# Performance work log

Measured on AMD Instinct MI355X. Metric: run time of the kernel, lower is better.

Reference implementation:

```python
import jax, jax.numpy as jnp
import numpy as np

B, N, C, NT = 32, 512, 32, 24   # batch, frames, channels-per-token, tokens
H, DH = 8, 48                   # heads, dim_head (DH % NT == 0 -> CS = 2)
E = H * DH                      # encode_dim = 384
IN = C * NT                     # in_dim = 768
OUT = 768                       # out_dim


def setup_inputs() -> dict:
    key = jax.random.key(0)
    ks = jax.random.split(key, 12)
    s = lambda fan_in: 1.0 / np.sqrt(fan_in)
    return {
        "x": jax.random.normal(ks[0], (B, N, C, NT), dtype=jnp.float32),
        "Wqkv_t": jax.random.uniform(ks[1], (IN, 3 * E), jnp.float32, -s(IN), s(IN)),
        "bqkv_t": jax.random.uniform(ks[2], (3 * E,), jnp.float32, -s(IN), s(IN)),
        "Wqkv_s": jax.random.uniform(ks[3], (IN, 3 * E), jnp.float32, -s(IN), s(IN)),
        "bqkv_s": jax.random.uniform(ks[4], (3 * E,), jnp.float32, -s(IN), s(IN)),
        "Wts": jax.random.uniform(ks[5], (2 * E, 2 * E), jnp.float32, -s(2 * E), s(2 * E)),
        "bts": jax.random.uniform(ks[6], (2 * E,), jnp.float32, -s(2 * E), s(2 * E)),
        "Wfc_t": jax.random.uniform(ks[7], (E, OUT), jnp.float32, -s(E), s(E)),
        "bfc_t": jax.random.uniform(ks[8], (OUT,), jnp.float32, -s(E), s(E)),
        "Wfc_s": jax.random.uniform(ks[9], (E, OUT), jnp.float32, -s(E), s(E)),
        "bfc_s": jax.random.uniform(ks[10], (OUT,), jnp.float32, -s(E), s(E)),
    }


def reference(x, Wqkv_t, bqkv_t, Wqkv_s, bqkv_s, Wts, bts, Wfc_t, bfc_t, Wfc_s, bfc_s):
    b, n, c, nt = x.shape
    cs = DH // nt  # channels per token inside a head (=2)
    xf = x.reshape(b, n, c * nt)                       # (b, n, in_dim)

    # --- temporal attention over the n (frame) axis ---
    qkv_t = (xf @ Wqkv_t + bqkv_t).reshape(b, n, 3, H, DH)
    qkv_t = jnp.transpose(qkv_t, (2, 0, 3, 1, 4))      # (3, b, H, n, DH)
    qt, kt, vt = qkv_t[0], qkv_t[1], qkv_t[2]
    attn_t = jax.nn.softmax(
        jnp.einsum('bhnd,bhmd->bhnm', qt, kt) / jnp.sqrt(jnp.float32(DH)), axis=-1)
    x_t = jnp.einsum('bhnm,bhmd->bnhd', attn_t, vt).reshape(b, n, E)

    # --- spatial attention over the nt (token) axis (note: unscaled, per source) ---
    qkv_s = (xf @ Wqkv_s + bqkv_s).reshape(b, n, 3, H, DH)
    qkv_s = jnp.transpose(qkv_s, (2, 0, 1, 3, 4)).reshape(3, b * n, H, cs, nt)
    qs, ks_, vs = qkv_s[0], qkv_s[1], qkv_s[2]         # (b*n, H, cs, nt)
    attn_s = jax.nn.softmax(jnp.einsum('ghct,ghcu->ghtu', qs, ks_), axis=-1)
    x_s = jnp.einsum('ghtu,ghcu->ghct', attn_s, vs)     # (b*n, H, cs, nt)
    x_s = x_s.reshape(b * n, H, cs * nt).reshape(b, n, E)

    # --- learned gating fusion ---
    alpha = jnp.concatenate([x_t, x_s], axis=-1).mean(axis=1, keepdims=True)  # (b,1,2E)
    alpha = (alpha @ Wts + bts).reshape(b, 1, E, 2)
    alpha = jax.nn.softmax(alpha, axis=-1)
    y = (x_t * alpha[:, :, :, 0]) @ Wfc_t + bfc_t + (x_s * alpha[:, :, :, 1]) @ Wfc_s + bfc_s
    return y  # dropout is identity in inference
```

## Files before the change

kernel.cpp:

```cpp
#include <hip/hip_runtime.h>
#include <hip/hip_bf16.h>


typedef __attribute__((ext_vector_type(8))) short s16x8;
typedef __attribute__((ext_vector_type(4))) float f32x4;

__device__ __forceinline__ float lo2f(uint u) { return __uint_as_float(u << 16); }
__device__ __forceinline__ float hi2f(uint u) { return __uint_as_float(u & 0xffff0000u); }
__device__ __forceinline__ ushort f2bu(float f) {
    union { __hip_bfloat16 h; ushort u; } c; c.h = __float2bfloat16(f); return c.u;
}
__device__ __forceinline__ uint pk2(float a, float b) {
    return (uint)f2bu(a) | ((uint)f2bu(b) << 16);
}
__device__ __forceinline__ void gload16(const void* g, void* l) {
    __builtin_amdgcn_global_load_lds((const __attribute__((address_space(1))) void*)g,
                                     (__attribute__((address_space(3))) void*)l, 16, 0, 0);
}

__global__ __launch_bounds__(256) void convert_bf16(
    const float* __restrict__ in, ushort* __restrict__ out)
{
    const int i = blockIdx.x * 256 + threadIdx.x;
    const float4* p = (const float4*)in + (size_t)i * 2;
    float4 a = p[0], b = p[1];
    uint4 o;
    o.x = pk2(a.x, a.y); o.y = pk2(a.z, a.w);
    o.z = pk2(b.x, b.y); o.w = pk2(b.z, b.w);
    ((uint4*)out)[i] = o;
}

__global__ __launch_bounds__(256) void concat_bias(
    const float* __restrict__ a, const float* __restrict__ b, float* __restrict__ o)
{
    const int i = blockIdx.x * 256 + threadIdx.x;
    o[i] = (i < 1152) ? a[i] : b[i - 1152];
}

__global__ __launch_bounds__(256) void transpose_w(
    const float* __restrict__ W, ushort* __restrict__ Bt,
    int K, int N, int Kt, int koff, int noff)
{
    __shared__ float t[32][33];
    const int k0 = blockIdx.x * 32, n0 = blockIdx.y * 32;
    const int r = threadIdx.x >> 3, cq = threadIdx.x & 7;
    float4 v = *(const float4*)(W + (size_t)(k0 + r) * N + n0 + cq * 4);
    t[r][cq * 4 + 0] = v.x; t[r][cq * 4 + 1] = v.y;
    t[r][cq * 4 + 2] = v.z; t[r][cq * 4 + 3] = v.w;
    __syncthreads();
    ushort4 o;
    o.x = f2bu(t[cq * 4 + 0][r]); o.y = f2bu(t[cq * 4 + 1][r]);
    o.z = f2bu(t[cq * 4 + 2][r]); o.w = f2bu(t[cq * 4 + 3][r]);
    *(ushort4*)(Bt + (size_t)(noff + n0 + r) * Kt + koff + k0 + cq * 4) = o;
}

template<int OUTBF16, int NBIAS>
__global__ __launch_bounds__(256, 2) void gemm128p(
    const ushort* __restrict__ A, const ushort* __restrict__ Bt,
    const float* __restrict__ bias0, const float* __restrict__ bias1,
    void* __restrict__ Cout, int M, int N, int K)
{
    __shared__ ushort smem[32768];
    const int tid = threadIdx.x;
    const int m0 = blockIdx.x * 128;
    const int n0 = blockIdx.y * 128;
    const int lane = tid & 63;
    const int wr = tid >> 7;
    const int wc = (tid >> 6) & 1;
    const int lr = lane & 15;
    const int g = lane >> 4;

    f32x4 acc[4][4];
#pragma unroll
    for (int i = 0; i < 4; ++i)
#pragma unroll
        for (int j = 0; j < 4; ++j) acc[i][j] = (f32x4){0.f, 0.f, 0.f, 0.f};

    int rowT[4], kqs[4];
#pragma unroll
    for (int i = 0; i < 4; ++i) {
        const int task = tid + 256 * i;
        rowT[i] = task >> 3;
        kqs[i] = (task & 7) ^ (rowT[i] & 7);
    }

    auto stage = [&](int buf, int k0) {
        ushort* dA = &smem[buf * 16384];
        ushort* dB = &smem[buf * 16384 + 8192];
#pragma unroll
        for (int i = 0; i < 4; ++i) {
            gload16(A + (size_t)(m0 + rowT[i]) * K + k0 + (kqs[i] << 3),
                    dA + (tid + 256 * i) * 8);
            gload16(Bt + (size_t)(n0 + rowT[i]) * K + k0 + (kqs[i] << 3),
                    dB + (tid + 256 * i) * 8);
        }
    };

    stage(0, 0);
    const int nt = K >> 6;
    for (int t = 0; t < nt; ++t) {
        const int cur = t & 1;
        if (t + 1 < nt) {
            stage(cur ^ 1, (t + 1) << 6);
            asm volatile("s_waitcnt vmcnt(8)" ::: "memory");
        } else {
            asm volatile("s_waitcnt vmcnt(0)" ::: "memory");
        }
        __builtin_amdgcn_sched_barrier(0);
        __builtin_amdgcn_s_barrier();
        __builtin_amdgcn_sched_barrier(0);

        const ushort* As = &smem[cur * 16384];
        const ushort* Bs = &smem[cur * 16384 + 8192];
#pragma unroll
        for (int half = 0; half < 2; ++half) {
            s16x8 af[4], bfv[4];
#pragma unroll
            for (int i = 0; i < 4; ++i) {
                const int row = wr * 64 + 16 * i + lr;
                af[i] = *(const s16x8*)&As[row * 64
                         + (((4 * half + g) ^ (row & 7)) << 3)];
            }
#pragma unroll
            for (int j = 0; j < 4; ++j) {
                const int row = wc * 64 + 16 * j + lr;
                bfv[j] = *(const s16x8*)&Bs[row * 64
                          + (((4 * half + g) ^ (row & 7)) << 3)];
            }
#pragma unroll
            for (int i = 0; i < 4; ++i)
#pragma unroll
                for (int j = 0; j < 4; ++j)
                    acc[i][j] = __builtin_amdgcn_mfma_f32_16x16x32_bf16(
                        af[i], bfv[j], acc[i][j], 0, 0, 0);
        }
        __builtin_amdgcn_sched_barrier(0);
        __builtin_amdgcn_s_barrier();
    }

    const int c0 = n0 + wc * 64 + lr;
    float bsum[4];
#pragma unroll
    for (int j = 0; j < 4; ++j) {
        bsum[j] = bias0[c0 + 16 * j];
        if (NBIAS == 2) bsum[j] += bias1[c0 + 16 * j];
    }
    const int r0 = m0 + wr * 64 + g * 4;
#pragma unroll
    for (int i = 0; i < 4; ++i) {
        const int row = r0 + 16 * i;
#pragma unroll
        for (int j = 0; j < 4; ++j) {
            const int col = c0 + 16 * j;
#pragma unroll
            for (int v = 0; v < 4; ++v) {
                const float val = acc[i][j][v] + bsum[j];
                if (OUTBF16)
                    ((ushort*)Cout)[(size_t)(row + v) * N + col] = f2bu(val);
                else
                    ((float*)Cout)[(size_t)(row + v) * N + col] = val;
            }
        }
    }
}

__global__ __launch_bounds__(256, 4) void attn_temporal(
    const ushort* __restrict__ qkv, ushort* __restrict__ xcat)
{
    const int wg = blockIdx.x;
    const int cx = wg & 7, rx = wg >> 3;
    const int id = ((rx >> 2) << 5) + 4 * cx + (rx & 3);
    const int qt = id & 3;
    const int h = (id >> 2) & 7;
    const int b = id >> 5;

    const int tid = threadIdx.x;
    const int w = tid >> 6;
    const int lane = tid & 63;
    const int lr = lane & 15;
    const int g = lane >> 4;

    __shared__ ushort Ks[64 * 64];
    __shared__ ushort Vt[48 * 64];
    __shared__ ushort Pl[4][32 * 72];
    uint* KsU = (uint*)Ks;
    uint* VtU = (uint*)Vt;

    ((uint4*)Ks)[tid] = make_uint4(0u, 0u, 0u, 0u);
    ((uint4*)Ks)[256 + tid] = make_uint4(0u, 0u, 0u, 0u);
    __syncthreads();

    const uint* qkvu = (const uint*)qkv;
    const int qrow0 = qt * 128 + w * 32;

    s16x8 qf[2][2];
#pragma unroll
    for (int n = 0; n < 2; ++n) {
        const size_t rb = (size_t)(b * 512 + qrow0 + 16 * n + lr) * 2304 + h * 48 + 8 * g;
        qf[n][0] = *(const s16x8*)(qkv + rb);
        qf[n][1] = (g < 2) ? *(const s16x8*)(qkv + rb + 32)
                           : (s16x8){0, 0, 0, 0, 0, 0, 0, 0};
    }

    int p_[3], du_[3];
#pragma unroll
    for (int i = 0; i < 3; ++i) {
        const int idx = tid + 256 * i;
        p_[i] = idx / 24;
        du_[i] = idx % 24;
    }
    uint rk[3][2], rv[3][2];

    auto stage_load = [&](int kv0) {
#pragma unroll
        for (int i = 0; i < 3; ++i) {
            const uint* s0 = qkvu + (size_t)(b * 512 + kv0 + 2 * p_[i]) * 1152
                                  + 192 + h * 24 + du_[i];
            rk[i][0] = s0[0];    rk[i][1] = s0[1152];
            rv[i][0] = s0[192];  rv[i][1] = s0[192 + 1152];
        }
    };
    auto stage_write = [&]() {
#pragma unroll
        for (int i = 0; i < 3; ++i) {
            const int p = p_[i], du = du_[i];
            KsU[(2 * p) * 32 + ((((du >> 2) ^ ((2 * p) & 7)) << 2) | (du & 3))] = rk[i][0];
            KsU[(2 * p + 1) * 32 + ((((du >> 2) ^ ((2 * p + 1) & 7)) << 2) | (du & 3))] = rk[i][1];
            const uint w0 = (rv[i][0] & 0xffffu) | (rv[i][1] << 16);
            const uint w1 = (rv[i][0] >> 16) | (rv[i][1] & 0xffff0000u);
            const int vb = (((p >> 2) ^ (du & 7)) << 2) | (p & 3);
            VtU[(2 * du) * 32 + vb] = w0;
            VtU[(2 * du + 1) * 32 + vb] = w1;
        }
    };

    f32x4 o[2][3];
#pragma unroll
    for (int mq = 0; mq < 2; ++mq)
#pragma unroll
        for (int nd = 0; nd < 3; ++nd) o[mq][nd] = (f32x4){0.f, 0.f, 0.f, 0.f};
    float mrun[2] = {-3.0e38f, -3.0e38f};
    float lsum[2] = {0.f, 0.f};
    float corrv[2];
    const float scale = 0.14433756729740643f;

    stage_load(0);
    stage_write();
    __syncthreads();

    for (int t = 0; t < 8; ++t) {
        if (t < 7) stage_load((t + 1) * 64);

        f32x4 sa[4][2];
#pragma unroll
        for (int m = 0; m < 4; ++m)
#pragma unroll
            for (int n = 0; n < 2; ++n) sa[m][n] = (f32x4){0.f, 0.f, 0.f, 0.f};
#pragma unroll
        for (int ks = 0; ks < 2; ++ks)
#pragma unroll
            for (int m = 0; m < 4; ++m) {
                s16x8 kf = *(const s16x8*)&Ks[(16 * m + lr) * 64
                                              + (((g + 4 * ks) ^ (lr & 7)) << 3)];
#pragma unroll
                for (int n = 0; n < 2; ++n)
                    sa[m][n] = __builtin_amdgcn_mfma_f32_16x16x32_bf16(
                        kf, qf[n][ks], sa[m][n], 0, 0, 0);
            }

#pragma unroll
        for (int n = 0; n < 2; ++n) {
            float tmax = -3.0e38f;
#pragma unroll
            for (int m = 0; m < 4; ++m)
#pragma unroll
                for (int v = 0; v < 4; ++v) tmax = fmaxf(tmax, sa[m][n][v]);
            tmax = fmaxf(tmax, __shfl_xor(tmax, 16));
            tmax = fmaxf(tmax, __shfl_xor(tmax, 32));
            float mnew = fmaxf(mrun[n], tmax * scale);
            float corr = __expf(mrun[n] - mnew);
            mrun[n] = mnew;
            float psum = 0.f;
#pragma unroll
            for (int m = 0; m < 4; ++m) {
                float p0 = __expf(fmaf(sa[m][n][0], scale, -mnew));
                float p1 = __expf(fmaf(sa[m][n][1], scale, -mnew));
                float p2 = __expf(fmaf(sa[m][n][2], scale, -mnew));
                float p3 = __expf(fmaf(sa[m][n][3], scale, -mnew));
                psum += (p0 + p1) + (p2 + p3);
                const int base = (16 * n + lr) * 72 + 16 * m + 4 * g;
                *(uint*)&Pl[w][base] = pk2(p0, p1);
                *(uint*)&Pl[w][base + 2] = pk2(p2, p3);
            }
            psum += __shfl_xor(psum, 16);
            psum += __shfl_xor(psum, 32);
            lsum[n] = lsum[n] * corr + psum;
            corrv[n] = corr;
        }

#pragma unroll
        for (int mq = 0; mq < 2; ++mq)
#pragma unroll
            for (int nd = 0; nd < 3; ++nd)
#pragma unroll
                for (int v = 0; v < 4; ++v) o[mq][nd][v] *= corrv[mq];

#pragma unroll
        for (int ks = 0; ks < 2; ++ks) {
            s16x8 vf[3];
#pragma unroll
            for (int nd = 0; nd < 3; ++nd)
                vf[nd] = *(const s16x8*)&Vt[(16 * nd + lr) * 64
                                            + (((g + 4 * ks) ^ (lr >> 1)) << 3)];
#pragma unroll
            for (int mq = 0; mq < 2; ++mq) {
                s16x8 pf = *(const s16x8*)&Pl[w][(16 * mq + lr) * 72 + 8 * g + 32 * ks];
#pragma unroll
                for (int nd = 0; nd < 3; ++nd)
                    o[mq][nd] = __builtin_amdgcn_mfma_f32_16x16x32_bf16(
                        vf[nd], pf, o[mq][nd], 0, 0, 0);
            }
        }
        __syncthreads();
        if (t < 7) stage_write();
        __syncthreads();
    }

#pragma unroll
    for (int mq = 0; mq < 2; ++mq) {
        const float li = 1.f / lsum[mq];
        const int qrow = qrow0 + 16 * mq + lr;
        ushort* dst = xcat + (size_t)(b * 512 + qrow) * 768 + h * 48;
#pragma unroll
        for (int nd = 0; nd < 3; ++nd) {
            uint2 o2;
            o2.x = pk2(o[mq][nd][0] * li, o[mq][nd][1] * li);
            o2.y = pk2(o[mq][nd][2] * li, o[mq][nd][3] * li);
            *(uint2*)(dst + 16 * nd + 4 * g) = o2;
        }
    }
}

__global__ __launch_bounds__(192) void attn_spatial(
    const ushort* __restrict__ qkv, ushort* __restrict__ xcat)
{
    const int g = blockIdx.x;
    __shared__ float row[1152];
    const uint* qkvu = (const uint*)qkv;
#pragma unroll
    for (int i = 0; i < 3; ++i) {
        int idx = threadIdx.x + 192 * i;
        uint u = qkvu[(size_t)g * 1152 + 576 + idx];
        row[2 * idx] = lo2f(u); row[2 * idx + 1] = hi2f(u);
    }
    __syncthreads();

    const int h = threadIdx.x / 24;
    const int t = threadIdx.x % 24;
    const float* q = &row[h * 48];
    const float* k = &row[384 + h * 48];
    const float* v = &row[768 + h * 48];
    const float q0 = q[t], q1 = q[24 + t];

    float s[24];
    float mx = -3.0e38f;
#pragma unroll
    for (int u = 0; u < 24; ++u) {
        s[u] = q0 * k[u] + q1 * k[24 + u];
        mx = fmaxf(mx, s[u]);
    }
    float l = 0.f;
#pragma unroll
    for (int u = 0; u < 24; ++u) { s[u] = __expf(s[u] - mx); l += s[u]; }
    const float inv = 1.f / l;
    float o0 = 0.f, o1 = 0.f;
#pragma unroll
    for (int u = 0; u < 24; ++u) {
        o0 = fmaf(s[u], v[u], o0);
        o1 = fmaf(s[u], v[24 + u], o1);
    }
    ushort* dst = xcat + (size_t)g * 768 + 384 + h * 48;
    dst[t] = f2bu(o0 * inv);
    dst[24 + t] = f2bu(o1 * inv);
}

__global__ __launch_bounds__(256) void colsum(
    const ushort* __restrict__ xcat, float* __restrict__ partial)
{
    const int b = blockIdx.x, ch = blockIdx.y, part = blockIdx.z;
    const int e = ch * 256 + threadIdx.x;
    const int n0 = part * 64;
    float s = 0.f;
    for (int n = 0; n < 64; ++n)
        s += __uint_as_float((uint)xcat[((size_t)(b * 512 + n0 + n)) * 768 + e] << 16);
    partial[((size_t)(b * 8 + part)) * 768 + e] = s;
}

__global__ __launch_bounds__(256) void alpha_gate(
    const float* __restrict__ partial, const float* __restrict__ Wts,
    const float* __restrict__ bts, float* __restrict__ gate)
{
    const int b = blockIdx.x;
    const int j0 = blockIdx.y * 128;
    __shared__ float av[768];
    __shared__ float psum[2][128];

    for (int i = threadIdx.x; i < 768; i += 256) {
        float s = 0.f;
#pragma unroll
        for (int p = 0; p < 8; ++p)
            s += partial[((size_t)(b * 8 + p)) * 768 + i];
        av[i] = s * (1.0f / 512.0f);
    }
    __syncthreads();

    const int jl = threadIdx.x & 127;
    const int seg = threadIdx.x >> 7;
    const int j = j0 + jl;
    const float* Wp = Wts + (size_t)(seg * 384) * 768 + j;
    const float* avp = av + seg * 384;
    float a0 = 0.f, a1 = 0.f, a2 = 0.f, a3 = 0.f;
    float a4 = 0.f, a5 = 0.f, a6 = 0.f, a7 = 0.f;
#pragma unroll 4
    for (int k = 0; k < 384; k += 8) {
        a0 = fmaf(avp[k + 0], Wp[(size_t)(k + 0) * 768], a0);
        a1 = fmaf(avp[k + 1], Wp[(size_t)(k + 1) * 768], a1);
        a2 = fmaf(avp[k + 2], Wp[(size_t)(k + 2) * 768], a2);
        a3 = fmaf(avp[k + 3], Wp[(size_t)(k + 3) * 768], a3);
        a4 = fmaf(avp[k + 4], Wp[(size_t)(k + 4) * 768], a4);
        a5 = fmaf(avp[k + 5], Wp[(size_t)(k + 5) * 768], a5);
        a6 = fmaf(avp[k + 6], Wp[(size_t)(k + 6) * 768], a6);
        a7 = fmaf(avp[k + 7], Wp[(size_t)(k + 7) * 768], a7);
    }
    psum[seg][jl] = ((a0 + a1) + (a2 + a3)) + ((a4 + a5) + (a6 + a7));
    __syncthreads();

    if (threadIdx.x < 128)
        av[threadIdx.x] = psum[0][threadIdx.x] + psum[1][threadIdx.x]
                        + bts[j0 + threadIdx.x];
    __syncthreads();
    if (threadIdx.x < 64) {
        const int e = (j0 >> 1) + threadIdx.x;
        float x0 = av[2 * threadIdx.x], x1 = av[2 * threadIdx.x + 1];
        float m = fmaxf(x0, x1);
        float e0 = __expf(x0 - m), e1 = __expf(x1 - m);
        float inv = 1.f / (e0 + e1);
        gate[(size_t)b * 768 + e] = e0 * inv;
        gate[(size_t)b * 768 + 384 + e] = e1 * inv;
    }
}

__global__ __launch_bounds__(256) void gate_mul(
    const ushort* __restrict__ xcat, const float* __restrict__ gate,
    ushort* __restrict__ xg)
{
    const int i = blockIdx.x * 256 + threadIdx.x;
    const int m = i / 96;
    const int k = (i % 96) * 8;
    const int b = m >> 9;
    uint4 u = ((const uint4*)xcat)[i];
    const float* g = gate + (size_t)b * 768 + k;
    float4 g0 = *(const float4*)g;
    float4 g1 = *(const float4*)(g + 4);
    uint4 o;
    o.x = pk2(lo2f(u.x) * g0.x, hi2f(u.x) * g0.y);
    o.y = pk2(lo2f(u.y) * g0.z, hi2f(u.y) * g0.w);
    o.z = pk2(lo2f(u.z) * g1.x, hi2f(u.z) * g1.y);
    o.w = pk2(lo2f(u.w) * g1.z, hi2f(u.w) * g1.w);
    ((uint4*)xg)[i] = o;
}

extern "C" void kernel_launch(void* const* d_in, const int* in_sizes, int n_in,
                              void* d_out, int out_size, void* d_ws, size_t ws_size,
                              hipStream_t stream)
{
    const float* x      = (const float*)d_in[0];
    const float* Wqkv_t = (const float*)d_in[1];
    const float* bqkv_t = (const float*)d_in[2];
    const float* Wqkv_s = (const float*)d_in[3];
    const float* bqkv_s = (const float*)d_in[4];
    const float* Wts    = (const float*)d_in[5];
    const float* bts    = (const float*)d_in[6];
    const float* Wfc_t  = (const float*)d_in[7];
    const float* bfc_t  = (const float*)d_in[8];
    const float* Wfc_s  = (const float*)d_in[9];
    const float* bfc_s  = (const float*)d_in[10];
    float* out = (float*)d_out;

    char* w = (char*)d_ws;
    ushort* qkv2   = (ushort*)(w);
    ushort* xg     = qkv2;
    ushort* xcat   = (ushort*)(w + 75497472);
    ushort* xb     = (ushort*)(w + 100663296);
    ushort* wbuf   = (ushort*)(w + 125829120);
    ushort* wbuf2  = (ushort*)(w + 129368064);
    float*  partial= (float*)(w + 130547712);
    float*  gate   = (float*)(w + 131334144);
    float*  bias2  = (float*)(w + 131432448);

    const dim3 blk256(256);

    convert_bf16<<<dim3(6144), blk256, 0, stream>>>(x, xb);
    concat_bias<<<dim3(9), blk256, 0, stream>>>(bqkv_t, bqkv_s, bias2);
    transpose_w<<<dim3(24, 36), blk256, 0, stream>>>(Wqkv_t, wbuf, 768, 1152, 768, 0, 0);
    transpose_w<<<dim3(24, 36), blk256, 0, stream>>>(Wqkv_s, wbuf, 768, 1152, 768, 0, 1152);

    gemm128p<1, 1><<<dim3(128, 18), blk256, 0, stream>>>(
        xb, wbuf, bias2, nullptr, qkv2, 16384, 2304, 768);

    attn_temporal<<<dim3(1024), blk256, 0, stream>>>(qkv2, xcat);
    attn_spatial<<<dim3(16384), dim3(192), 0, stream>>>(qkv2, xcat);

    colsum<<<dim3(32, 3, 8), blk256, 0, stream>>>(xcat, partial);
    alpha_gate<<<dim3(32, 6), blk256, 0, stream>>>(partial, Wts, bts, gate);
    gate_mul<<<dim3(6144), blk256, 0, stream>>>(xcat, gate, xg);

    transpose_w<<<dim3(12, 24), blk256, 0, stream>>>(Wfc_t, wbuf2, 384, 768, 768, 0, 0);
    transpose_w<<<dim3(12, 24), blk256, 0, stream>>>(Wfc_s, wbuf2, 384, 768, 768, 384, 0);
    gemm128p<0, 2><<<dim3(128, 6), blk256, 0, stream>>>(
        xg, wbuf2, bfc_t, bfc_s, out, 16384, 768, 768);
}
```

Measured before the change: 200.5 us.

## Restage GEMM in fragment-ordered k-halves and raise MFMA wave priority

The GEMM now loads each 64-wide k-tile as two 32-wide halves written to shared memory directly in MFMA fragment order, so each lane reads its operand with one contiguous 16-byte load and no XOR swizzle. The next tile's halves are issued at two separate points inside the loop, giving a finer load/compute pipeline. s_setprio is raised around MFMA bursts in both the GEMM and the temporal attention kernel so waves in their matrix phase are favoured by the scheduler. The cost is more barriers per iteration, and the contiguous layout may introduce LDS bank conflicts on the global-to-LDS writes.

```diff
diff --git a/kernel.cpp b/kernel.cpp
--- a/kernel.cpp
+++ b/kernel.cpp
@@ -55,15 +55,15 @@
 }
 
 template<int OUTBF16, int NBIAS>
-__global__ __launch_bounds__(256, 2) void gemm128p(
+__global__ __launch_bounds__(256, 2) void gemm128q(
     const ushort* __restrict__ A, const ushort* __restrict__ Bt,
     const float* __restrict__ bias0, const float* __restrict__ bias1,
     void* __restrict__ Cout, int M, int N, int K)
 {
     __shared__ ushort smem[32768];
     const int tid = threadIdx.x;
-    const int m0 = blockIdx.x * 128;
-    const int n0 = blockIdx.y * 128;
+    const int m0 = blockIdx.x << 7;
+    const int n0 = blockIdx.y << 7;
     const int lane = tid & 63;
     const int wr = tid >> 7;
     const int wc = (tid >> 6) & 1;
@@ -76,32 +76,67 @@
 #pragma unroll
         for (int j = 0; j < 4; ++j) acc[i][j] = (f32x4){0.f, 0.f, 0.f, 0.f};
 
-    int rowT[4], kqs[4];
-#pragma unroll
-    for (int i = 0; i < 4; ++i) {
-        const int task = tid + 256 * i;
-        rowT[i] = task >> 3;
-        kqs[i] = (task & 7) ^ (rowT[i] & 7);
-    }
-
-    auto stage = [&](int buf, int k0) {
-        ushort* dA = &smem[buf * 16384];
-        ushort* dB = &smem[buf * 16384 + 8192];
-#pragma unroll
-        for (int i = 0; i < 4; ++i) {
-            gload16(A + (size_t)(m0 + rowT[i]) * K + k0 + (kqs[i] << 3),
-                    dA + (tid + 256 * i) * 8);
-            gload16(Bt + (size_t)(n0 + rowT[i]) * K + k0 + (kqs[i] << 3),
-                    dB + (tid + 256 * i) * 8);
-        }
+    int rowS[2], chS[2];
+#pragma unroll
+    for (int i = 0; i < 2; ++i) {
+        const int s = tid + 256 * i;
+        rowS[i] = ((s >> 6) << 4) | (s & 15);
+        chS[i] = (s >> 4) & 3;
+    }
+
+    auto stage = [&](const ushort* P, int rbase, int k0, int lb) {
+#pragma unroll
+        for (int i = 0; i < 2; ++i)
+            gload16(P + (size_t)(rbase + rowS[i]) * K + k0 + (chS[i] << 3),
+                    &smem[lb + (tid + 256 * i) * 8]);
     };
 
-    stage(0, 0);
+    stage(A, m0, 0, 0);
+    stage(Bt, n0, 0, 8192);
+    stage(A, m0, 32, 4096);
+    stage(Bt, n0, 32, 12288);
+
     const int nt = K >> 6;
     for (int t = 0; t < nt; ++t) {
-        const int cur = t & 1;
-        if (t + 1 < nt) {
-            stage(cur ^ 1, (t + 1) << 6);
+        const int db = (t & 1) * 16384;
+        const int pb = db ^ 16384;
+        const bool pf = (t + 1) < nt;
+        const int kn = (t + 1) << 6;
+
+        if (pf) {
+            stage(A, m0, kn, pb);
+            stage(Bt, n0, kn, pb + 8192);
+            asm volatile("s_waitcnt vmcnt(8)" ::: "memory");
+        } else {
+            asm volatile("s_waitcnt vmcnt(4)" ::: "memory");
+        }
+        __builtin_amdgcn_sched_barrier(0);
+        __builtin_amdgcn_s_barrier();
+        __builtin_amdgcn_sched_barrier(0);
+        {
+            s16x8 af[4], bf[4];
+#pragma unroll
+            for (int i = 0; i < 4; ++i)
+                af[i] = *(const s16x8*)&smem[db + (wr * 4 + i) * 512 + lane * 8];
+#pragma unroll
+            for (int j = 0; j < 4; ++j)
+                bf[j] = *(const s16x8*)&smem[db + 8192 + (wc * 4 + j) * 512 + lane * 8];
+            __builtin_amdgcn_s_setprio(1);
+#pragma unroll
+            for (int i = 0; i < 4; ++i)
+#pragma unroll
+                for (int j = 0; j < 4; ++j)
+                    acc[i][j] = __builtin_amdgcn_mfma_f32_16x16x32_bf16(
+                        af[i], bf[j], acc[i][j], 0, 0, 0);
+            __builtin_amdgcn_s_setprio(0);
+        }
+        __builtin_amdgcn_sched_barrier(0);
+        __builtin_amdgcn_s_barrier();
+        __builtin_amdgcn_sched_barrier(0);
+
+        if (pf) {
+            stage(A, m0, kn + 32, pb + 4096);
+            stage(Bt, n0, kn + 32, pb + 12288);
             asm volatile("s_waitcnt vmcnt(8)" ::: "memory");
         } else {
             asm volatile("s_waitcnt vmcnt(0)" ::: "memory");
@@ -109,33 +144,26 @@
         __builtin_amdgcn_sched_barrier(0);
         __builtin_amdgcn_s_barrier();
         __builtin_amdgcn_sched_barrier(0);
-
-        const ushort* As = &smem[cur * 16384];
-        const ushort* Bs = &smem[cur * 16384 + 8192];
-#pragma unroll
-        for (int half = 0; half < 2; ++half) {
-            s16x8 af[4], bfv[4];
-#pragma unroll
-            for (int i = 0; i < 4; ++i) {
-                const int row = wr * 64 + 16 * i + lr;
-                af[i] = *(const s16x8*)&As[row * 64
-                         + (((4 * half + g) ^ (row & 7)) << 3)];
-            }
-#pragma unroll
-            for (int j = 0; j < 4; ++j) {
-                const int row = wc * 64 + 16 * j + lr;
-                bfv[j] = *(const s16x8*)&Bs[row * 64
-                          + (((4 * half + g) ^ (row & 7)) << 3)];
-            }
+        {
+            s16x8 af[4], bf[4];
+#pragma unroll
+            for (int i = 0; i < 4; ++i)
+                af[i] = *(const s16x8*)&smem[db + 4096 + (wr * 4 + i) * 512 + lane * 8];
+#pragma unroll
+            for (int j = 0; j < 4; ++j)
+                bf[j] = *(const s16x8*)&smem[db + 12288 + (wc * 4 + j) * 512 + lane * 8];
+            __builtin_amdgcn_s_setprio(1);
 #pragma unroll
             for (int i = 0; i < 4; ++i)
 #pragma unroll
                 for (int j = 0; j < 4; ++j)
                     acc[i][j] = __builtin_amdgcn_mfma_f32_16x16x32_bf16(
-                        af[i], bfv[j], acc[i][j], 0, 0, 0);
+                        af[i], bf[j], acc[i][j], 0, 0, 0);
+            __builtin_amdgcn_s_setprio(0);
         }
         __builtin_amdgcn_sched_barrier(0);
         __builtin_amdgcn_s_barrier();
+        __builtin_amdgcn_sched_barrier(0);
     }
 
     const int c0 = n0 + wc * 64 + lr;
@@ -256,6 +284,7 @@
         for (int m = 0; m < 4; ++m)
 #pragma unroll
             for (int n = 0; n < 2; ++n) sa[m][n] = (f32x4){0.f, 0.f, 0.f, 0.f};
+        __builtin_amdgcn_s_setprio(1);
 #pragma unroll
         for (int ks = 0; ks < 2; ++ks)
 #pragma unroll
@@ -267,6 +296,7 @@
                     sa[m][n] = __builtin_amdgcn_mfma_f32_16x16x32_bf16(
                         kf, qf[n][ks], sa[m][n], 0, 0, 0);
             }
+        __builtin_amdgcn_s_setprio(0);
 
 #pragma unroll
         for (int n = 0; n < 2; ++n) {
@@ -305,6 +335,7 @@
 #pragma unroll
                 for (int v = 0; v < 4; ++v) o[mq][nd][v] *= corrv[mq];
 
+        __builtin_amdgcn_s_setprio(1);
 #pragma unroll
         for (int ks = 0; ks < 2; ++ks) {
             s16x8 vf[3];
@@ -321,6 +352,7 @@
                         vf[nd], pf, o[mq][nd], 0, 0, 0);
             }
         }
+        __builtin_amdgcn_s_setprio(0);
         __syncthreads();
         if (t < 7) stage_write();
         __syncthreads();
@@ -505,7 +537,7 @@
     transpose_w<<<dim3(24, 36), blk256, 0, stream>>>(Wqkv_t, wbuf, 768, 1152, 768, 0, 0);
     transpose_w<<<dim3(24, 36), blk256, 0, stream>>>(Wqkv_s, wbuf, 768, 1152, 768, 0, 1152);
 
-    gemm128p<1, 1><<<dim3(128, 18), blk256, 0, stream>>>(
+    gemm128q<1, 1><<<dim3(128, 18), blk256, 0, stream>>>(
         xb, wbuf, bias2, nullptr, qkv2, 16384, 2304, 768);
 
     attn_temporal<<<dim3(1024), blk256, 0, stream>>>(qkv2, xcat);
@@ -517,6 +549,6 @@
 
     transpose_w<<<dim3(12, 24), blk256, 0, stream>>>(Wfc_t, wbuf2, 384, 768, 768, 0, 0);
     transpose_w<<<dim3(12, 24), blk256, 0, stream>>>(Wfc_s, wbuf2, 384, 768, 768, 384, 0);
-    gemm128p<0, 2><<<dim3(128, 6), blk256, 0, stream>>>(
+    gemm128q<0, 2><<<dim3(128, 6), blk256, 0, stream>>>(
         xg, wbuf2, bfc_t, bfc_s, out, 16384, 768, 768);
 }
```

New measurement: 252.7 us. 26.0% more time.

## Shrink GEMM K-tile to 32 with fragment-ordered LDS layout and MFMA priority

Applied to the files above, without the earlier changes.

The GEMM now stages 32-wide K slices, half the previous 64, into a smaller shared buffer. Data is laid out in LDS so each lane reads its MFMA fragment as one contiguous 16-byte chunk, which removes the XOR swizzle address math, and launch bounds are raised to allow 4 blocks per CU. The MFMA sections in the GEMM and temporal attention are wrapped in s_setprio so matrix work gets issue priority. The cost is twice as many K iterations and barriers per tile, and higher register pressure at the raised occupancy target could cause spills.

```diff
diff --git a/kernel.cpp b/kernel.cpp
--- a/kernel.cpp
+++ b/kernel.cpp
@@ -55,15 +55,15 @@
 }
 
 template<int OUTBF16, int NBIAS>
-__global__ __launch_bounds__(256, 2) void gemm128p(
+__global__ __launch_bounds__(256, 4) void gemm128s(
     const ushort* __restrict__ A, const ushort* __restrict__ Bt,
     const float* __restrict__ bias0, const float* __restrict__ bias1,
     void* __restrict__ Cout, int M, int N, int K)
 {
-    __shared__ ushort smem[32768];
+    __shared__ ushort smem[16384];
     const int tid = threadIdx.x;
-    const int m0 = blockIdx.x * 128;
-    const int n0 = blockIdx.y * 128;
+    const int m0 = blockIdx.x << 7;
+    const int n0 = blockIdx.y << 7;
     const int lane = tid & 63;
     const int wr = tid >> 7;
     const int wc = (tid >> 6) & 1;
@@ -76,33 +76,34 @@
 #pragma unroll
         for (int j = 0; j < 4; ++j) acc[i][j] = (f32x4){0.f, 0.f, 0.f, 0.f};
 
-    int rowT[4], kqs[4];
-#pragma unroll
-    for (int i = 0; i < 4; ++i) {
-        const int task = tid + 256 * i;
-        rowT[i] = task >> 3;
-        kqs[i] = (task & 7) ^ (rowT[i] & 7);
+    int rowS[2], chS[2];
+#pragma unroll
+    for (int i = 0; i < 2; ++i) {
+        const int s = tid + 256 * i;
+        rowS[i] = ((s >> 6) << 4) | (s & 15);
+        chS[i] = (s >> 4) & 3;
     }
 
     auto stage = [&](int buf, int k0) {
-        ushort* dA = &smem[buf * 16384];
-        ushort* dB = &smem[buf * 16384 + 8192];
-#pragma unroll
-        for (int i = 0; i < 4; ++i) {
-            gload16(A + (size_t)(m0 + rowT[i]) * K + k0 + (kqs[i] << 3),
+        ushort* dA = &smem[buf * 8192];
+        ushort* dB = &smem[buf * 8192 + 4096];
+#pragma unroll
+        for (int i = 0; i < 2; ++i)
+            gload16(A + (size_t)(m0 + rowS[i]) * K + k0 + (chS[i] << 3),
                     dA + (tid + 256 * i) * 8);
-            gload16(Bt + (size_t)(n0 + rowT[i]) * K + k0 + (kqs[i] << 3),
+#pragma unroll
+        for (int i = 0; i < 2; ++i)
+            gload16(Bt + (size_t)(n0 + rowS[i]) * K + k0 + (chS[i] << 3),
                     dB + (tid + 256 * i) * 8);
-        }
     };
 
     stage(0, 0);
-    const int nt = K >> 6;
+    const int nt = K >> 5;
     for (int t = 0; t < nt; ++t) {
         const int cur = t & 1;
         if (t + 1 < nt) {
-            stage(cur ^ 1, (t + 1) << 6);
-            asm volatile("s_waitcnt vmcnt(8)" ::: "memory");
+            stage(cur ^ 1, (t + 1) << 5);
+            asm volatile("s_waitcnt vmcnt(4)" ::: "memory");
         } else {
             asm volatile("s_waitcnt vmcnt(0)" ::: "memory");
         }
@@ -110,30 +111,23 @@
         __builtin_amdgcn_s_barrier();
         __builtin_amdgcn_sched_barrier(0);
 
-        const ushort* As = &smem[cur * 16384];
-        const ushort* Bs = &smem[cur * 16384 + 8192];
-#pragma unroll
-        for (int half = 0; half < 2; ++half) {
-            s16x8 af[4], bfv[4];
-#pragma unroll
-            for (int i = 0; i < 4; ++i) {
-                const int row = wr * 64 + 16 * i + lr;
-                af[i] = *(const s16x8*)&As[row * 64
-                         + (((4 * half + g) ^ (row & 7)) << 3)];
-            }
-#pragma unroll
-            for (int j = 0; j < 4; ++j) {
-                const int row = wc * 64 + 16 * j + lr;
-                bfv[j] = *(const s16x8*)&Bs[row * 64
-                          + (((4 * half + g) ^ (row & 7)) << 3)];
-            }
-#pragma unroll
-            for (int i = 0; i < 4; ++i)
-#pragma unroll
-                for (int j = 0; j < 4; ++j)
-                    acc[i][j] = __builtin_amdgcn_mfma_f32_16x16x32_bf16(
-                        af[i], bfv[j], acc[i][j], 0, 0, 0);
-        }
+        const ushort* As = &smem[cur * 8192];
+        const ushort* Bs = &smem[cur * 8192 + 4096];
+        s16x8 af[4], bf[4];
+#pragma unroll
+        for (int i = 0; i < 4; ++i)
+            af[i] = *(const s16x8*)&As[(wr * 4 + i) * 512 + lane * 8];
+#pragma unroll
+        for (int j = 0; j < 4; ++j)
+            bf[j] = *(const s16x8*)&Bs[(wc * 4 + j) * 512 + lane * 8];
+        __builtin_amdgcn_s_setprio(1);
+#pragma unroll
+        for (int i = 0; i < 4; ++i)
+#pragma unroll
+            for (int j = 0; j < 4; ++j)
+                acc[i][j] = __builtin_amdgcn_mfma_f32_16x16x32_bf16(
+                    af[i], bf[j], acc[i][j], 0, 0, 0);
+        __builtin_amdgcn_s_setprio(0);
         __builtin_amdgcn_sched_barrier(0);
         __builtin_amdgcn_s_barrier();
     }
@@ -256,6 +250,7 @@
         for (int m = 0; m < 4; ++m)
 #pragma unroll
             for (int n = 0; n < 2; ++n) sa[m][n] = (f32x4){0.f, 0.f, 0.f, 0.f};
+        __builtin_amdgcn_s_setprio(1);
 #pragma unroll
         for (int ks = 0; ks < 2; ++ks)
 #pragma unroll
@@ -267,6 +262,7 @@
                     sa[m][n] = __builtin_amdgcn_mfma_f32_16x16x32_bf16(
                         kf, qf[n][ks], sa[m][n], 0, 0, 0);
             }
+        __builtin_amdgcn_s_setprio(0);
 
 #pragma unroll
         for (int n = 0; n < 2; ++n) {
@@ -305,6 +301,7 @@
 #pragma unroll
                 for (int v = 0; v < 4; ++v) o[mq][nd][v] *= corrv[mq];
 
+        __builtin_amdgcn_s_setprio(1);
 #pragma unroll
         for (int ks = 0; ks < 2; ++ks) {
             s16x8 vf[3];
@@ -321,6 +318,7 @@
                         vf[nd], pf, o[mq][nd], 0, 0, 0);
             }
         }
+        __builtin_amdgcn_s_setprio(0);
         __syncthreads();
         if (t < 7) stage_write();
         __syncthreads();
@@ -505,7 +503,7 @@
     transpose_w<<<dim3(24, 36), blk256, 0, stream>>>(Wqkv_t, wbuf, 768, 1152, 768, 0, 0);
     transpose_w<<<dim3(24, 36), blk256, 0, stream>>>(Wqkv_s, wbuf, 768, 1152, 768, 0, 1152);
 
-    gemm128p<1, 1><<<dim3(128, 18), blk256, 0, stream>>>(
+    gemm128s<1, 1><<<dim3(128, 18), blk256, 0, stream>>>(
         xb, wbuf, bias2, nullptr, qkv2, 16384, 2304, 768);
 
     attn_temporal<<<dim3(1024), blk256, 0, stream>>>(qkv2, xcat);
@@ -517,6 +515,6 @@
 
     transpose_w<<<dim3(12, 24), blk256, 0, stream>>>(Wfc_t, wbuf2, 384, 768, 768, 0, 0);
     transpose_w<<<dim3(12, 24), blk256, 0, stream>>>(Wfc_s, wbuf2, 384, 768, 768, 384, 0);
-    gemm128p<0, 2><<<dim3(128, 6), blk256, 0, stream>>>(
+    gemm128s<0, 2><<<dim3(128, 6), blk256, 0, stream>>>(
         xg, wbuf2, bfc_t, bfc_s, out, 16384, 768, 768);
 }
```

New measurement: 252.5 us. 1.26x slower.

## Merge input conversion, bias concat and weight transposes into one prep kernel; add MFMA priority

Applied to the files above, without the earlier changes.

Six small preprocessing launches (x to bf16, bias concat, four weight transposes) become one kernel that picks its job from the block index, so launch gaps go away and the small transposes run alongside the large conversion. The temporal attention kernel also raises wave priority with s_setprio around its two MFMA loops, so matrix work is scheduled ahead of other waves. The transpose blocks now share one shared-memory tile declaration, and the setprio hints may not help depending on how waves interleave.

```diff
diff --git a/kernel.cpp b/kernel.cpp
--- a/kernel.cpp
+++ b/kernel.cpp
@@ -18,31 +18,12 @@
                                      (__attribute__((address_space(3))) void*)l, 16, 0, 0);
 }
 
-__global__ __launch_bounds__(256) void convert_bf16(
-    const float* __restrict__ in, ushort* __restrict__ out)
-{
-    const int i = blockIdx.x * 256 + threadIdx.x;
-    const float4* p = (const float4*)in + (size_t)i * 2;
-    float4 a = p[0], b = p[1];
-    uint4 o;
-    o.x = pk2(a.x, a.y); o.y = pk2(a.z, a.w);
-    o.z = pk2(b.x, b.y); o.w = pk2(b.z, b.w);
-    ((uint4*)out)[i] = o;
-}
-
-__global__ __launch_bounds__(256) void concat_bias(
-    const float* __restrict__ a, const float* __restrict__ b, float* __restrict__ o)
-{
-    const int i = blockIdx.x * 256 + threadIdx.x;
-    o[i] = (i < 1152) ? a[i] : b[i - 1152];
-}
-
-__global__ __launch_bounds__(256) void transpose_w(
+__device__ __forceinline__ void transpose_blk(
     const float* __restrict__ W, ushort* __restrict__ Bt,
-    int K, int N, int Kt, int koff, int noff)
-{
-    __shared__ float t[32][33];
-    const int k0 = blockIdx.x * 32, n0 = blockIdx.y * 32;
+    int task, int KT, int N, int Kt, int koff, int noff, float (*t)[33])
+{
+    const int k0 = (task % KT) * 32;
+    const int n0 = (task / KT) * 32;
     const int r = threadIdx.x >> 3, cq = threadIdx.x & 7;
     float4 v = *(const float4*)(W + (size_t)(k0 + r) * N + n0 + cq * 4);
     t[r][cq * 4 + 0] = v.x; t[r][cq * 4 + 1] = v.y;
@@ -52,6 +33,39 @@
     o.x = f2bu(t[cq * 4 + 0][r]); o.y = f2bu(t[cq * 4 + 1][r]);
     o.z = f2bu(t[cq * 4 + 2][r]); o.w = f2bu(t[cq * 4 + 3][r]);
     *(ushort4*)(Bt + (size_t)(noff + n0 + r) * Kt + koff + k0 + cq * 4) = o;
+}
+
+__global__ __launch_bounds__(256) void prep(
+    const float* __restrict__ x, ushort* __restrict__ xb,
+    const float* __restrict__ bqkv_t, const float* __restrict__ bqkv_s,
+    float* __restrict__ bias2,
+    const float* __restrict__ Wqkv_t, const float* __restrict__ Wqkv_s,
+    ushort* __restrict__ wbuf,
+    const float* __restrict__ Wfc_t, const float* __restrict__ Wfc_s,
+    ushort* __restrict__ wbuf2)
+{
+    __shared__ float t[32][33];
+    const int bid = blockIdx.x;
+    if (bid < 6144) {
+        const int i = bid * 256 + threadIdx.x;
+        const float4* p = (const float4*)x + (size_t)i * 2;
+        float4 a = p[0], b = p[1];
+        uint4 o;
+        o.x = pk2(a.x, a.y); o.y = pk2(a.z, a.w);
+        o.z = pk2(b.x, b.y); o.w = pk2(b.z, b.w);
+        ((uint4*)xb)[i] = o;
+    } else if (bid < 6153) {
+        const int i = (bid - 6144) * 256 + threadIdx.x;
+        bias2[i] = (i < 1152) ? bqkv_t[i] : bqkv_s[i - 1152];
+    } else if (bid < 7017) {
+        transpose_blk(Wqkv_t, wbuf, bid - 6153, 24, 1152, 768, 0, 0, t);
+    } else if (bid < 7881) {
+        transpose_blk(Wqkv_s, wbuf, bid - 7017, 24, 1152, 768, 0, 1152, t);
+    } else if (bid < 8169) {
+        transpose_blk(Wfc_t, wbuf2, bid - 7881, 12, 768, 768, 0, 0, t);
+    } else {
+        transpose_blk(Wfc_s, wbuf2, bid - 8169, 12, 768, 768, 384, 0, t);
+    }
 }
 
 template<int OUTBF16, int NBIAS>
@@ -256,6 +270,7 @@
         for (int m = 0; m < 4; ++m)
 #pragma unroll
             for (int n = 0; n < 2; ++n) sa[m][n] = (f32x4){0.f, 0.f, 0.f, 0.f};
+        __builtin_amdgcn_s_setprio(1);
 #pragma unroll
         for (int ks = 0; ks < 2; ++ks)
 #pragma unroll
@@ -267,6 +282,7 @@
                     sa[m][n] = __builtin_amdgcn_mfma_f32_16x16x32_bf16(
                         kf, qf[n][ks], sa[m][n], 0, 0, 0);
             }
+        __builtin_amdgcn_s_setprio(0);
 
 #pragma unroll
         for (int n = 0; n < 2; ++n) {
@@ -305,6 +321,7 @@
 #pragma unroll
                 for (int v = 0; v < 4; ++v) o[mq][nd][v] *= corrv[mq];
 
+        __builtin_amdgcn_s_setprio(1);
 #pragma unroll
         for (int ks = 0; ks < 2; ++ks) {
             s16x8 vf[3];
@@ -321,6 +338,7 @@
                         vf[nd], pf, o[mq][nd], 0, 0, 0);
             }
         }
+        __builtin_amdgcn_s_setprio(0);
         __syncthreads();
         if (t < 7) stage_write();
         __syncthreads();
@@ -500,10 +518,8 @@
 
     const dim3 blk256(256);
 
-    convert_bf16<<<dim3(6144), blk256, 0, stream>>>(x, xb);
-    concat_bias<<<dim3(9), blk256, 0, stream>>>(bqkv_t, bqkv_s, bias2);
-    transpose_w<<<dim3(24, 36), blk256, 0, stream>>>(Wqkv_t, wbuf, 768, 1152, 768, 0, 0);
-    transpose_w<<<dim3(24, 36), blk256, 0, stream>>>(Wqkv_s, wbuf, 768, 1152, 768, 0, 1152);
+    prep<<<dim3(8457), blk256, 0, stream>>>(
+        x, xb, bqkv_t, bqkv_s, bias2, Wqkv_t, Wqkv_s, wbuf, Wfc_t, Wfc_s, wbuf2);
 
     gemm128p<1, 1><<<dim3(128, 18), blk256, 0, stream>>>(
         xb, wbuf, bias2, nullptr, qkv2, 16384, 2304, 768);
@@ -515,8 +531,6 @@
     alpha_gate<<<dim3(32, 6), blk256, 0, stream>>>(partial, Wts, bts, gate);
     gate_mul<<<dim3(6144), blk256, 0, stream>>>(xcat, gate, xg);
 
-    transpose_w<<<dim3(12, 24), blk256, 0, stream>>>(Wfc_t, wbuf2, 384, 768, 768, 0, 0);
-    transpose_w<<<dim3(12, 24), blk256, 0, stream>>>(Wfc_s, wbuf2, 384, 768, 768, 384, 0);
     gemm128p<0, 2><<<dim3(128, 6), blk256, 0, stream>>>(
         xg, wbuf2, bfc_t, bfc_s, out, 16384, 768, 768);
 }
```

Measured after the change: 190.4 us. -5.0%, faster.
